# Kernel optimization log

Measured on AMD Instinct MI355X. Metric: run time of the kernel, lower is better.

The kernel has to match this reference:

```python
import jax, jax.numpy as jnp
import numpy as np

N, E, B = 100000, 400000, 4096      # nodes, directed edges, graphs
P, d = 4, 49                        # phm_dim, per-component dim; D = P*d = 196
L = 3                               # message-passing layers
D1, D2 = 64, 32                     # downstream per-component dims (256/4, 128/4)


def setup_inputs():
    key = jax.random.key(0)
    ks = jax.random.split(key, 20)
    def nrm(k, shape, s=0.1):
        return jax.random.normal(k, shape, dtype=jnp.float32) * s
    return {
        "x": jax.random.randint(ks[0], (N, 9), 0, 119),
        "edge_index": jax.random.randint(ks[1], (2, E), 0, N),
        "edge_attr": jax.random.randint(ks[2], (E, 3), 0, 8),
        "batch": jnp.sort(jax.random.randint(ks[3], (N,), 0, B)),
        # encoders: summed categorical embeddings in hypercomplex form [*, P, d]
        "atom_emb": nrm(ks[4], (9, 119, P, d)),
        "bond_emb": nrm(ks[5], (L, 3, 8, P, d)),
        # per-layer PHM conv: contribution matrices A (phm rule) + component weights W
        "conv_A": nrm(ks[6], (L, P, P, P), 0.5),
        "conv_W": nrm(ks[7], (L, P, d, d)),
        "conv_b": jnp.zeros((L, P, d), jnp.float32),
        "mp_gamma": jnp.ones((L, P * d), jnp.float32),
        "mp_beta": jnp.zeros((L, P * d), jnp.float32),
        # soft-attention pooling: PHM linear + real transformer gate
        "pool_A": nrm(ks[8], (P, P, P), 0.5),
        "pool_W": nrm(ks[9], (P, d, d)),
        "pool_b": jnp.zeros((P, d), jnp.float32),
        "pool_rt_w": nrm(ks[10], (P,), 0.5),
        "pool_rt_b": jnp.zeros((d,), jnp.float32),
        # downstream PHM MLP 196 -> 256 -> 128 -> 4*1, then real trafo -> 1
        "dn_A": nrm(ks[11], (3, P, P, P), 0.5),
        "dn1_W": nrm(ks[12], (P, d, D1)),
        "dn1_b": jnp.zeros((P, D1), jnp.float32),
        "dn1_gamma": jnp.ones((P * D1,), jnp.float32),
        "dn1_beta": jnp.zeros((P * D1,), jnp.float32),
        "dn2_W": nrm(ks[13], (P, D1, D2)),
        "dn2_b": jnp.zeros((P, D2), jnp.float32),
        "dn2_gamma": jnp.ones((P * D2,), jnp.float32),
        "dn2_beta": jnp.zeros((P * D2,), jnp.float32),
        "dn3_W": nrm(ks[14], (P, D2, 1)),
        "dn3_b": jnp.zeros((P, 1), jnp.float32),
        "rt_w": nrm(ks[15], (P,), 0.5),
        "rt_b": jnp.zeros((1,), jnp.float32),
    }


def phm_linear(x, A, W, b):
    # PHM linear: y = x @ (sum_i kron(A_i, W_i)) + b, on [n, P, din] -> [n, P, dout]
    return jnp.einsum('nkp,ikj,ipq->njq', x, A, W) + b


def naive_bn(x, gamma, beta, eps=1e-5):
    # naive batch norm over the batch axis, per flattened hypercomplex feature
    n, p, dd = x.shape
    x2 = x.reshape(n, p * dd)
    mu = x2.mean(axis=0)
    var = x2.var(axis=0)
    x2 = (x2 - mu) * jax.lax.rsqrt(var + eps) * gamma + beta
    return x2.reshape(n, p, dd)


def reference(x, edge_index, edge_attr, batch, atom_emb, bond_emb,
              conv_A, conv_W, conv_b, mp_gamma, mp_beta,
              pool_A, pool_W, pool_b, pool_rt_w, pool_rt_b,
              dn_A, dn1_W, dn1_b, dn1_gamma, dn1_beta,
              dn2_W, dn2_b, dn2_gamma, dn2_beta, dn3_W, dn3_b, rt_w, rt_b):
    src, dst = edge_index[0], edge_index[1]
    # atom encoder: sum embeddings of 9 categorical features -> [N, P, d]
    h0 = atom_emb[jnp.arange(9), x].sum(axis=1)
    h = h0
    for l in range(L):  # small fixed layer count
        # bond encoder for this layer -> [E, P, d]
        e = bond_emb[l][jnp.arange(3), edge_attr].sum(axis=1)
        # message = x_j + e_ij (identity msg encoder); self-loop (zero edge feat) adds h
        m = h[src] + e
        agg = jax.ops.segment_sum(m, dst, num_segments=N) + h
        z = phm_linear(agg, conv_A[l], conv_W[l], conv_b[l])
        z = jax.nn.relu(naive_bn(z, mp_gamma[l], mp_beta[l]))
        h = z + h0  # skip-connect to first embedding (sc_type='first')
    # soft-attention pooling: real-valued sigmoid gate per node feature
    g = jax.nn.sigmoid(
        jnp.einsum('npk,p->nk', phm_linear(h, pool_A, pool_W, pool_b), pool_rt_w)
        + pool_rt_b)
    pooled = jax.ops.segment_sum(h * g[:, None, :], batch, num_segments=B)  # [B, P, d]
    # downstream PHM MLP with naive batch norm + relu
    z = jax.nn.relu(naive_bn(phm_linear(pooled, dn_A[0], dn1_W, dn1_b), dn1_gamma, dn1_beta))
    z = jax.nn.relu(naive_bn(phm_linear(z, dn_A[1], dn2_W, dn2_b), dn2_gamma, dn2_beta))
    o = phm_linear(z, dn_A[2], dn3_W, dn3_b)          # [B, P, 1]
    return jnp.einsum('npk,p->nk', o, rt_w) + rt_b    # [B, 1]
```

## Files before the change

### kernel.cpp

```cpp
#include <hip/hip_runtime.h>
#include <cstdint>
#include <cstddef>

#define N_NODES 100000
#define N_EDGES 400000
#define N_GRAPHS 4096
#define DF 196
#define DD 49
#define NPB 5
#define TST 200
#define WSLOT 14336
#define EST 232

#define AS1 __attribute__((address_space(1)))
#define AS3 __attribute__((address_space(3)))

typedef __bf16 bf16x8 __attribute__((ext_vector_type(8)));
typedef float f32x4 __attribute__((ext_vector_type(4)));

__device__ __forceinline__ unsigned short f2bf(float f) {
  unsigned int u = __float_as_uint(f);
  u = u + 0x7FFFu + ((u >> 16) & 1u);
  return (unsigned short)(u >> 16);
}
__device__ __forceinline__ float bf2f(unsigned short h) {
  return __uint_as_float(((unsigned int)h) << 16);
}

__global__ void convert_wfrag_kernel(const float* __restrict__ cA,
                                     const float* __restrict__ cW,
                                     unsigned short* __restrict__ wfrag) {
  int idx = blockIdx.x * blockDim.x + threadIdx.x;
  if (idx >= 3 * 100352) return;
  int l = idx / 100352;
  int r = idx - l * 100352;
  int ct = r / 7168; int r1 = r - ct * 7168;
  int ks = r1 / 1024; int r2 = r1 - ks * 1024;
  int h = r2 / 512;  int r3 = r2 - h * 512;
  int ln = r3 / 8;   int j = r3 - ln * 8;
  int col = ct * 16 + (ln & 15);
  int k = ks * 32 + (ln >> 4) * 8 + j;
  float v = 0.f;
  if (col < DF && k < DF) {
    int k4 = k / DD, p = k - (k / DD) * DD;
    int j4 = col / DD, q = col - (col / DD) * DD;
#pragma unroll
    for (int i = 0; i < 4; i++)
      v += cA[((l * 4 + i) * 4 + k4) * 4 + j4] * cW[((l * 4 + i) * DD + p) * DD + q];
  }
  unsigned short hi = f2bf(v);
  wfrag[idx] = (h == 0) ? hi : f2bf(v - bf2f(hi));
}

__global__ void setup_small_kernel(const float* __restrict__ bond, float* __restrict__ lut,
                                   const float* __restrict__ pA, const float* __restrict__ pW,
                                   const float* __restrict__ pb, const float* __restrict__ rtw,
                                   const float* __restrict__ rtb,
                                   float* __restrict__ gateW, float* __restrict__ gbias,
                                   const float* __restrict__ dnA,
                                   const float* __restrict__ W1, const float* __restrict__ W2,
                                   const float* __restrict__ W3,
                                   float* __restrict__ M1, float* __restrict__ M2,
                                   float* __restrict__ M3) {
  int idx0 = blockIdx.x * blockDim.x + threadIdx.x;
  const int NL = 3 * 512 * DF;
  const int NG = DF * DD + DD;
  const int n1 = DF * 256, n2 = 256 * 128, n3 = 128 * 4;
  if (idx0 < NL) {
    int idx = idx0;
    int l = idx / (512 * DF);
    int r = idx - l * (512 * DF);
    int code = r / DF, c = r - (r / DF) * DF;
    int a0 = code & 7, a1 = (code >> 3) & 7, a2 = (code >> 6) & 7;
    lut[idx] = bond[((l * 3 + 0) * 8 + a0) * DF + c]
             + bond[((l * 3 + 1) * 8 + a1) * DF + c]
             + bond[((l * 3 + 2) * 8 + a2) * DF + c];
  } else if (idx0 < NL + NG) {
    int idx = idx0 - NL;
    if (idx < DF * DD) {
      int r = idx / DD, q = idx - (idx / DD) * DD;
      int k = r / DD, p = r - (r / DD) * DD;
      float s = 0.f;
#pragma unroll
      for (int i = 0; i < 4; i++) {
        float aw = 0.f;
#pragma unroll
        for (int j = 0; j < 4; j++) aw += pA[(i * 4 + k) * 4 + j] * rtw[j];
        s += aw * pW[(i * DD + p) * DD + q];
      }
      gateW[idx] = s;
    } else {
      int q = idx - DF * DD;
      float s = rtb[q];
#pragma unroll
      for (int j = 0; j < 4; j++) s += rtw[j] * pb[j * DD + q];
      gbias[q] = s;
    }
  } else if (idx0 < NL + NG + n1 + n2 + n3) {
    int idx = idx0 - NL - NG;
    if (idx < n1) {
      int r = idx >> 8, c = idx & 255;
      int k = r / DD, p = r - (r / DD) * DD;
      int j = c >> 6, Q = c & 63;
      float s = 0.f;
#pragma unroll
      for (int i = 0; i < 4; i++) s += dnA[i * 16 + k * 4 + j] * W1[(i * DD + p) * 64 + Q];
      M1[idx] = s;
    } else if (idx < n1 + n2) {
      int m = idx - n1;
      int r = m >> 7, c = m & 127;
      int k = r >> 6, p = r & 63, j = c >> 5, q = c & 31;
      float s = 0.f;
#pragma unroll
      for (int i = 0; i < 4; i++) s += dnA[64 + i * 16 + k * 4 + j] * W2[(i * 64 + p) * 32 + q];
      M2[m] = s;
    } else {
      int m = idx - n1 - n2;
      int r = m >> 2, j = m & 3;
      int k = r >> 5, p = r & 31;
      float s = 0.f;
#pragma unroll
      for (int i = 0; i < 4; i++) s += dnA[128 + i * 16 + k * 4 + j] * W3[i * 32 + p];
      M3[m] = s;
    }
  }
}

__global__ void hist_kernel(const int* __restrict__ dst, int* __restrict__ counts) {
  int e = blockIdx.x * blockDim.x + threadIdx.x;
  if (e < N_EDGES) atomicAdd(&counts[dst[e]], 1);
}

__global__ void scan_local_kernel(const int* __restrict__ counts, int* __restrict__ offs,
                                  int* __restrict__ bsum) {
  __shared__ int sm[256];
  int tid = threadIdx.x;
  int gid = blockIdx.x * 256 + tid;
  int v = (gid < N_NODES) ? counts[gid] : 0;
  sm[tid] = v;
  __syncthreads();
  for (int d = 1; d < 256; d <<= 1) {
    int add = (tid >= d) ? sm[tid - d] : 0;
    __syncthreads();
    sm[tid] += add;
    __syncthreads();
  }
  if (gid < N_NODES) offs[gid] = sm[tid] - v;
  if (tid == 255) bsum[blockIdx.x] = sm[255];
}

__global__ void scan_bsum_kernel(int* __restrict__ bsum, int* __restrict__ bpre, int nb) {
  __shared__ int sm[512];
  int tid = threadIdx.x;
  int v = (tid < nb) ? bsum[tid] : 0;
  sm[tid] = v;
  __syncthreads();
  for (int d = 1; d < 512; d <<= 1) {
    int add = (tid >= d) ? sm[tid - d] : 0;
    __syncthreads();
    sm[tid] += add;
    __syncthreads();
  }
  if (tid < nb) bpre[tid] = sm[tid] - v;
}

__global__ void add_off_kernel(int* __restrict__ offs, const int* __restrict__ bpre) {
  int gid = blockIdx.x * blockDim.x + threadIdx.x;
  if (gid < N_NODES) offs[gid] += bpre[gid >> 8];
  if (gid == 0) offs[N_NODES] = N_EDGES;
}

__global__ void scatter_kernel(const int* __restrict__ src, const int* __restrict__ dst,
                               const int* __restrict__ ea, int* __restrict__ counts,
                               const int* __restrict__ offs,
                               unsigned int* __restrict__ sorted) {
  int e = blockIdx.x * blockDim.x + threadIdx.x;
  if (e >= N_EDGES) return;
  int d = dst[e];
  int code = ea[e * 3 + 0] | (ea[e * 3 + 1] << 3) | (ea[e * 3 + 2] << 6);
  int pos = offs[d] + atomicSub(&counts[d], 1) - 1;
  sorted[pos] = (unsigned int)src[e] | ((unsigned int)code << 17);
}

__global__ void sortseg_kernel(const int* __restrict__ offs,
                               unsigned int* __restrict__ sorted) {
  int n = blockIdx.x * blockDim.x + threadIdx.x;
  if (n >= N_NODES) return;
  int s = offs[n], e = offs[n + 1];
  for (int i = s + 1; i < e; i++) {
    unsigned int v = sorted[i];
    int j = i - 1;
    while (j >= s && sorted[j] > v) { sorted[j + 1] = sorted[j]; j--; }
    sorted[j + 1] = v;
  }
}

__global__ void atom_enc_kernel(const int* __restrict__ x, const float* __restrict__ emb,
                                float* __restrict__ h0) {
  int idx = blockIdx.x * blockDim.x + threadIdx.x;
  if (idx >= N_NODES * DF) return;
  int n = idx / DF;
  int c = idx - n * DF;
  float s = 0.f;
#pragma unroll
  for (int f = 0; f < 9; f++) {
    int xi = x[n * 9 + f];
    s += emb[(f * 119 + xi) * DF + c];
  }
  h0[idx] = s;
}

__global__ __launch_bounds__(256)
void agg_kernel(const float* __restrict__ h, const int* __restrict__ offs,
                const unsigned int* __restrict__ sorted, const float* __restrict__ lut,
                unsigned short* __restrict__ tH, unsigned short* __restrict__ tL) {
  int t = threadIdx.x;
  int i = t / 49, q = t - i * 49;
  if (i >= NPB) return;
  int node = blockIdx.x * NPB + i;
  if (node >= N_NODES) return;
  const float4* h4 = (const float4*)h;
  const float4* l4 = (const float4*)lut;
  float4 acc = h4[(size_t)node * 49 + q];
  int s = offs[node], e = offs[node + 1];
  for (int k = s; k < e; k++) {
    unsigned int se = sorted[k];
    int srcn = se & 0x1FFFF;
    int code = se >> 17;
    float4 hv = h4[(size_t)srcn * 49 + q];
    float4 lv = l4[(size_t)code * 49 + q];
    acc.x += hv.x + lv.x;
    acc.y += hv.y + lv.y;
    acc.z += hv.z + lv.z;
    acc.w += hv.w + lv.w;
  }
  ushort4 hh, ll;
  hh.x = f2bf(acc.x); ll.x = f2bf(acc.x - bf2f(hh.x));
  hh.y = f2bf(acc.y); ll.y = f2bf(acc.y - bf2f(hh.y));
  hh.z = f2bf(acc.z); ll.z = f2bf(acc.z - bf2f(hh.z));
  hh.w = f2bf(acc.w); ll.w = f2bf(acc.w - bf2f(hh.w));
  size_t ob = (size_t)node * TST + q * 4;
  *(ushort4*)(tH + ob) = hh;
  *(ushort4*)(tL + ob) = ll;
  if (q == 48) {
    ushort4 z = make_ushort4(0, 0, 0, 0);
    *(ushort4*)(tH + (size_t)node * TST + 196) = z;
    *(ushort4*)(tL + (size_t)node * TST + 196) = z;
  }
}

__global__ __launch_bounds__(256, 2)
void conv_mfma_kernel(unsigned short* __restrict__ tH,
                      unsigned short* __restrict__ tL,
                      const unsigned short* __restrict__ wfrag,
                      const float* __restrict__ bias,
                      float* __restrict__ stats) {
  __shared__ __align__(16) unsigned short smW[2 * 64 * EST];
  const int t = threadIdx.x;
  const int lane = t & 63;
  const int w = t >> 6;
  const int li = lane & 15;
  const int rg = lane >> 4;
  const int rowbase = blockIdx.x * 128 + w * 32;

  f32x4 acc[2][14];
#pragma unroll
  for (int rt = 0; rt < 2; rt++)
#pragma unroll
    for (int ct = 0; ct < 14; ct++) acc[rt][ct] = (f32x4){0.f, 0.f, 0.f, 0.f};

  uint4 b0h[2], b0l[2], b1h[2], b1l[2], b2h[2], b2l[2], b3h[2], b3l[2];

#define LOADA(ks, aH, aL)                                                      \
  {                                                                            \
    _Pragma("unroll") for (int rt = 0; rt < 2; rt++) {                         \
      size_t o = (size_t)(rowbase + rt * 16 + li) * TST + (ks) * 32 + rg * 8;  \
      aH[rt] = *(const uint4*)(tH + o);                                        \
      aL[rt] = *(const uint4*)(tL + o);                                        \
    }                                                                          \
  }

#define WLOAD(ks, sbase)                                                       \
  {                                                                            \
    _Pragma("unroll") for (int f0 = 0; f0 < 7; f0++) {                         \
      int g = f0 * 4 + w;                                                      \
      int hh = g & 1, ct = g >> 1;                                             \
      __builtin_amdgcn_global_load_lds(                                        \
          (AS1 const void*)(wfrag + ((size_t)(ct * 7 + (ks)) * 2 + hh) * 512 + lane * 8), \
          (AS3 void*)(smW + (sbase) + (ct * 2 + hh) * 512), 16, 0, 0);         \
    }                                                                          \
  }

#define COMPUTE(sbase, aH, aL)                                                 \
  {                                                                            \
    _Pragma("unroll") for (int ct = 0; ct < 14; ct++) {                        \
      bf16x8 bh = *(const bf16x8*)(smW + (sbase) + ((ct * 2 + 0) * 512 + lane * 8)); \
      bf16x8 bl = *(const bf16x8*)(smW + (sbase) + ((ct * 2 + 1) * 512 + lane * 8)); \
      _Pragma("unroll") for (int rt = 0; rt < 2; rt++) {                       \
        bf16x8 ah = *(const bf16x8*)&aH[rt];                                   \
        bf16x8 al = *(const bf16x8*)&aL[rt];                                   \
        acc[rt][ct] = __builtin_amdgcn_mfma_f32_16x16x32_bf16(ah, bh, acc[rt][ct], 0, 0, 0); \
        acc[rt][ct] = __builtin_amdgcn_mfma_f32_16x16x32_bf16(al, bh, acc[rt][ct], 0, 0, 0); \
        acc[rt][ct] = __builtin_amdgcn_mfma_f32_16x16x32_bf16(ah, bl, acc[rt][ct], 0, 0, 0); \
      }                                                                        \
    }                                                                          \
  }

#define BARC(N)                                                                \
  {                                                                            \
    asm volatile("s_waitcnt vmcnt(" #N ")" ::: "memory");                      \
    __builtin_amdgcn_s_barrier();                                              \
  }
#define PINW() __builtin_amdgcn_sched_barrier(0)

  WLOAD(0, 0);
  PINW();
  LOADA(0, b0h, b0l);
  LOADA(1, b1h, b1l);
  LOADA(2, b2h, b2l);
  BARC(12);
  WLOAD(1, WSLOT); PINW(); LOADA(3, b3h, b3l); COMPUTE(0, b0h, b0l);     BARC(4);
  WLOAD(2, 0);     PINW(); LOADA(4, b0h, b0l); COMPUTE(WSLOT, b1h, b1l); BARC(4);
  WLOAD(3, WSLOT); PINW(); LOADA(5, b1h, b1l); COMPUTE(0, b2h, b2l);     BARC(4);
  WLOAD(4, 0);     PINW(); LOADA(6, b2h, b2l); COMPUTE(WSLOT, b3h, b3l); BARC(4);
  WLOAD(5, WSLOT); PINW();                     COMPUTE(0, b0h, b0l);     BARC(0);
  WLOAD(6, 0);     PINW();                     COMPUTE(WSLOT, b1h, b1l); BARC(0);
  COMPUTE(0, b2h, b2l);

  float part[14], psq[14];
#pragma unroll
  for (int ct = 0; ct < 14; ct++) { part[ct] = 0.f; psq[ct] = 0.f; }

  unsigned short* lhi = smW;
  unsigned short* llo = smW + 64 * EST;

#pragma unroll
  for (int half = 0; half < 2; half++) {
    __syncthreads();
    if ((w >> 1) == half) {
      int rl0 = (w & 1) * 32;
#pragma unroll
      for (int ct = 0; ct < 14; ct++) {
        int c = ct * 16 + li;
        float bv = (c < DF) ? bias[c] : 0.f;
#pragma unroll
        for (int rt = 0; rt < 2; rt++) {
#pragma unroll
          for (int r = 0; r < 4; r++) {
            int row = rl0 + rt * 16 + rg * 4 + r;
            int gr = rowbase + rt * 16 + rg * 4 + r;
            float y = acc[rt][ct][r] + bv;
            if (gr < N_NODES && c < DF) { part[ct] += y; psq[ct] += y * y; }
            unsigned short hi = f2bf(y);
            lhi[row * EST + c] = hi;
            llo[row * EST + c] = f2bf(y - bf2f(hi));
          }
        }
      }
    }
    __syncthreads();
    for (int idx = t; idx < 1600; idx += 256) {
      int row = idx / 25, u = idx - (idx / 25) * 25;
      int gr = blockIdx.x * 128 + half * 64 + row;
      if (gr < N_NODES) {
        uint4 vh = *(const uint4*)(lhi + row * EST + u * 8);
        uint4 vl = *(const uint4*)(llo + row * EST + u * 8);
        if (u == 24) { vh.z = 0u; vh.w = 0u; vl.z = 0u; vl.w = 0u; }
        *(uint4*)(tH + (size_t)gr * TST + u * 8) = vh;
        *(uint4*)(tL + (size_t)gr * TST + u * 8) = vl;
      }
    }
  }

  __syncthreads();
  float* redS = (float*)smW;
  float* redQ = redS + 4 * 224;
#pragma unroll
  for (int ct = 0; ct < 14; ct++) {
    float p = part[ct], q = psq[ct];
    p += __shfl_xor(p, 16, 64); p += __shfl_xor(p, 32, 64);
    q += __shfl_xor(q, 16, 64); q += __shfl_xor(q, 32, 64);
    if (rg == 0) { redS[w * 224 + ct * 16 + li] = p; redQ[w * 224 + ct * 16 + li] = q; }
  }
  __syncthreads();
  if (t < DF) {
    float s1 = redS[t] + redS[224 + t] + redS[448 + t] + redS[672 + t];
    float s2 = redQ[t] + redQ[224 + t] + redQ[448 + t] + redQ[672 + t];
    atomicAdd(&stats[t], s1);
    atomicAdd(&stats[DF + t], s2);
  }
#undef LOADA
#undef WLOAD
#undef COMPUTE
#undef BARC
#undef PINW
}

__global__ void bn_relu_split_kernel(const unsigned short* __restrict__ tH,
                                     const unsigned short* __restrict__ tL,
                                     const float* __restrict__ stats,
                                     const float* __restrict__ gamma,
                                     const float* __restrict__ beta,
                                     const float* __restrict__ h0,
                                     float* __restrict__ h) {
  int idx = blockIdx.x * blockDim.x + threadIdx.x;
  if (idx >= N_NODES * DD) return;
  int n = idx / DD, q = idx - (idx / DD) * DD;
  size_t ib = (size_t)n * TST + q * 4;
  ushort4 hv = *(const ushort4*)(tH + ib);
  ushort4 lv = *(const ushort4*)(tL + ib);
  size_t fb = (size_t)n * DF + q * 4;
  float4 sk = *(const float4*)(h0 + fb);
  int c = q * 4;
  const float invN = 1.f / N_NODES;
  float4 o;
  {
    float z = bf2f(hv.x) + bf2f(lv.x);
    float mu = stats[c + 0] * invN;
    float var = stats[DF + c + 0] * invN - mu * mu;
    o.x = fmaxf((z - mu) * rsqrtf(var + 1e-5f) * gamma[c + 0] + beta[c + 0], 0.f) + sk.x;
  }
  {
    float z = bf2f(hv.y) + bf2f(lv.y);
    float mu = stats[c + 1] * invN;
    float var = stats[DF + c + 1] * invN - mu * mu;
    o.y = fmaxf((z - mu) * rsqrtf(var + 1e-5f) * gamma[c + 1] + beta[c + 1], 0.f) + sk.y;
  }
  {
    float z = bf2f(hv.z) + bf2f(lv.z);
    float mu = stats[c + 2] * invN;
    float var = stats[DF + c + 2] * invN - mu * mu;
    o.z = fmaxf((z - mu) * rsqrtf(var + 1e-5f) * gamma[c + 2] + beta[c + 2], 0.f) + sk.z;
  }
  {
    float z = bf2f(hv.w) + bf2f(lv.w);
    float mu = stats[c + 3] * invN;
    float var = stats[DF + c + 3] * invN - mu * mu;
    o.w = fmaxf((z - mu) * rsqrtf(var + 1e-5f) * gamma[c + 3] + beta[c + 3], 0.f) + sk.w;
  }
  *(float4*)(h + fb) = o;
}

template<int S, int MODE>
__launch_bounds__(256)
__global__ void gemm_kernel(const float* X, const float* __restrict__ W,
                            const float* __restrict__ bias, float* Y,
                            float* __restrict__ stats, int Nrows, int K, int NC) {
  constexpr int WN = S * 64;
  __shared__ __align__(16) float At[32][64];
  __shared__ __align__(16) float Wl[32][WN];
  const int t = threadIdx.x;
  const int tx = t & 15;
  const int ty = t >> 4;
  const int r0 = blockIdx.x * 64;

  float acc[S][4][4];
#pragma unroll
  for (int s = 0; s < S; s++)
#pragma unroll
    for (int i = 0; i < 4; i++)
#pragma unroll
      for (int j = 0; j < 4; j++) acc[s][i][j] = 0.f;

  const int lr = t >> 2;
  const int kb = (t & 3) * 8;
  constexpr int TPR = S * 16;
  const int cw = (t % TPR) * 4;
  const int kr = t / TPR;
  constexpr int RPP = 256 / TPR;
  constexpr int PASSES = 32 / RPP;

  for (int k0 = 0; k0 < K; k0 += 32) {
    {
      const int gr = r0 + lr;
      const float* xp = X + (size_t)gr * K + k0 + kb;
      if (gr < Nrows && (k0 + kb + 7) < K) {
        float4 v0 = *(const float4*)(xp);
        float4 v1 = *(const float4*)(xp + 4);
        At[kb + 0][lr] = v0.x; At[kb + 1][lr] = v0.y;
        At[kb + 2][lr] = v0.z; At[kb + 3][lr] = v0.w;
        At[kb + 4][lr] = v1.x; At[kb + 5][lr] = v1.y;
        At[kb + 6][lr] = v1.z; At[kb + 7][lr] = v1.w;
      } else {
#pragma unroll
        for (int i = 0; i < 8; i++) {
          int kk = kb + i;
          float v = 0.f;
          if (gr < Nrows && (k0 + kk) < K) v = xp[i];
          At[kk][lr] = v;
        }
      }
    }
#pragma unroll
    for (int ps = 0; ps < PASSES; ps++) {
      int kk = kr + ps * RPP;
      int gk = k0 + kk;
      if (gk < K && (cw + 3) < NC && ((NC & 3) == 0)) {
        float4 v = *(const float4*)(W + (size_t)gk * NC + cw);
        Wl[kk][cw + 0] = v.x; Wl[kk][cw + 1] = v.y;
        Wl[kk][cw + 2] = v.z; Wl[kk][cw + 3] = v.w;
      } else {
#pragma unroll
        for (int j = 0; j < 4; j++) {
          int c = cw + j;
          float v = 0.f;
          if (gk < K && c < NC) v = W[(size_t)gk * NC + c];
          Wl[kk][c] = v;
        }
      }
    }
    __syncthreads();
#pragma unroll 4
    for (int kk = 0; kk < 32; kk++) {
      float4 a = *(const float4*)&At[kk][ty * 4];
      float av[4] = {a.x, a.y, a.z, a.w};
#pragma unroll
      for (int s = 0; s < S; s++) {
        float4 w = *(const float4*)&Wl[kk][s * 64 + tx * 4];
        float wv[4] = {w.x, w.y, w.z, w.w};
#pragma unroll
        for (int i = 0; i < 4; i++)
#pragma unroll
          for (int j = 0; j < 4; j++)
            acc[s][i][j] = fmaf(av[i], wv[j], acc[s][i][j]);
      }
    }
    __syncthreads();
  }

#pragma unroll
  for (int s = 0; s < S; s++)
#pragma unroll
    for (int j = 0; j < 4; j++) {
      int c = s * 64 + tx * 4 + j;
      float bv = (c < NC) ? bias[c] : 0.f;
#pragma unroll
      for (int i = 0; i < 4; i++) {
        float y = acc[s][i][j] + bv;
        if (MODE == 1) y = 1.f / (1.f + __expf(-y));
        acc[s][i][j] = y;
      }
    }
#pragma unroll
  for (int i = 0; i < 4; i++) {
    int gr = r0 + ty * 4 + i;
    if (gr < Nrows) {
#pragma unroll
      for (int s = 0; s < S; s++)
#pragma unroll
        for (int j = 0; j < 4; j++) {
          int c = s * 64 + tx * 4 + j;
          if (c < NC) Y[(size_t)gr * NC + c] = acc[s][i][j];
        }
    }
  }
  if (MODE == 0) {
    float* red = &Wl[0][0];
    __syncthreads();
#pragma unroll
    for (int s = 0; s < S; s++)
#pragma unroll
      for (int j = 0; j < 4; j++) {
        float p = 0.f;
#pragma unroll
        for (int i = 0; i < 4; i++)
          if ((r0 + ty * 4 + i) < Nrows) p += acc[s][i][j];
        red[ty * WN + s * 64 + tx * 4 + j] = p;
      }
    __syncthreads();
    if (t < WN) {
      float tot = 0.f;
#pragma unroll
      for (int yy = 0; yy < 16; yy++) tot += red[yy * WN + t];
      if (t < NC) atomicAdd(&stats[t], tot);
    }
    __syncthreads();
#pragma unroll
    for (int s = 0; s < S; s++)
#pragma unroll
      for (int j = 0; j < 4; j++) {
        float p = 0.f;
#pragma unroll
        for (int i = 0; i < 4; i++)
          if ((r0 + ty * 4 + i) < Nrows) p += acc[s][i][j] * acc[s][i][j];
        red[ty * WN + s * 64 + tx * 4 + j] = p;
      }
    __syncthreads();
    if (t < WN) {
      float tot = 0.f;
#pragma unroll
      for (int yy = 0; yy < 16; yy++) tot += red[yy * WN + t];
      if (t < NC) atomicAdd(&stats[NC + t], tot);
    }
  }
}

__global__ void bn_relu_kernel(const float* __restrict__ z, const float* __restrict__ stats,
                               const float* __restrict__ gamma, const float* __restrict__ beta,
                               float* __restrict__ out,
                               int total, int NC, float invN) {
  int idx = blockIdx.x * blockDim.x + threadIdx.x;
  if (idx >= total) return;
  int c = idx % NC;
  float mu = stats[c] * invN;
  float var = stats[NC + c] * invN - mu * mu;
  float v = (z[idx] - mu) * rsqrtf(var + 1e-5f) * gamma[c] + beta[c];
  out[idx] = fmaxf(v, 0.f);
}

__device__ __forceinline__ int lower_bound_dev(const int* a, int n, int v) {
  int lo = 0, hi = n;
  while (lo < hi) { int mid = (lo + hi) >> 1; if (a[mid] < v) lo = mid + 1; else hi = mid; }
  return lo;
}

__global__ void pool_kernel(const float* __restrict__ h, const float* __restrict__ g,
                            const int* __restrict__ batch, float* __restrict__ pooled) {
  int b = blockIdx.x;
  __shared__ int bounds[2];
  if (threadIdx.x == 0) {
    bounds[0] = lower_bound_dev(batch, N_NODES, b);
    bounds[1] = lower_bound_dev(batch, N_NODES, b + 1);
  }
  __syncthreads();
  int c = threadIdx.x;
  if (c >= DF) return;
  int s = bounds[0], e = bounds[1];
  int q = c % DD;
  float acc = 0.f;
  for (int n = s; n < e; n++)
    acc = fmaf(h[(size_t)n * DF + c], g[(size_t)n * DD + q], acc);
  pooled[(size_t)b * DF + c] = acc;
}

__global__ void final_kernel(const float* __restrict__ z2, const float* __restrict__ M3,
                             const float* __restrict__ b3, const float* __restrict__ rtw,
                             const float* __restrict__ rtb, float* __restrict__ out) {
  __shared__ float sM[128 * 4];
  __shared__ float srw[4];
  __shared__ float srb;
  int t = threadIdx.x;
  for (int i = t; i < 512; i += 256) sM[i] = M3[i];
  if (t < 4) srw[t] = rtw[t];
  if (t == 4) srb = rtb[0];
  __syncthreads();
  int b = blockIdx.x * blockDim.x + t;
  if (b >= N_GRAPHS) return;
  float o0 = b3[0], o1 = b3[1], o2 = b3[2], o3 = b3[3];
  const float* zp = z2 + (size_t)b * 128;
  for (int p = 0; p < 128; p++) {
    float v = zp[p];
    o0 = fmaf(v, sM[p * 4 + 0], o0);
    o1 = fmaf(v, sM[p * 4 + 1], o1);
    o2 = fmaf(v, sM[p * 4 + 2], o2);
    o3 = fmaf(v, sM[p * 4 + 3], o3);
  }
  out[b] = srb + o0 * srw[0] + o1 * srw[1] + o2 * srw[2] + o3 * srw[3];
}

extern "C" void kernel_launch(void* const* d_in, const int* in_sizes, int n_in,
                              void* d_out, int out_size, void* d_ws, size_t ws_size,
                              hipStream_t stream) {
  (void)in_sizes; (void)n_in; (void)out_size; (void)ws_size;
  const int* x          = (const int*)d_in[0];
  const int* edge_index = (const int*)d_in[1];
  const int* edge_attr  = (const int*)d_in[2];
  const int* batch      = (const int*)d_in[3];
  const float* atom_emb = (const float*)d_in[4];
  const float* bond_emb = (const float*)d_in[5];
  const float* conv_A   = (const float*)d_in[6];
  const float* conv_W   = (const float*)d_in[7];
  const float* conv_b   = (const float*)d_in[8];
  const float* mp_gamma = (const float*)d_in[9];
  const float* mp_beta  = (const float*)d_in[10];
  const float* pool_A   = (const float*)d_in[11];
  const float* pool_W   = (const float*)d_in[12];
  const float* pool_b   = (const float*)d_in[13];
  const float* pool_rt_w = (const float*)d_in[14];
  const float* pool_rt_b = (const float*)d_in[15];
  const float* dn_A     = (const float*)d_in[16];
  const float* dn1_W    = (const float*)d_in[17];
  const float* dn1_b    = (const float*)d_in[18];
  const float* dn1_gamma = (const float*)d_in[19];
  const float* dn1_beta = (const float*)d_in[20];
  const float* dn2_W    = (const float*)d_in[21];
  const float* dn2_b    = (const float*)d_in[22];
  const float* dn2_gamma = (const float*)d_in[23];
  const float* dn2_beta = (const float*)d_in[24];
  const float* dn3_W    = (const float*)d_in[25];
  const float* dn3_b    = (const float*)d_in[26];
  const float* rt_w     = (const float*)d_in[27];
  const float* rt_b     = (const float*)d_in[28];
  float* out = (float*)d_out;

  char* ws = (char*)d_ws;
  size_t off = 0;
  auto alloc = [&](size_t bytes) -> char* {
    char* p = ws + off;
    off = (off + bytes + 255) & ~(size_t)255;
    return p;
  };
  const size_t HBYTES = (size_t)N_NODES * DF * sizeof(float);
  float* h0 = (float*)alloc(HBYTES);
  float* h  = (float*)alloc(HBYTES);
  unsigned short* tH = (unsigned short*)alloc((size_t)N_NODES * TST * 2 + 4096);
  unsigned short* tL = (unsigned short*)alloc((size_t)N_NODES * TST * 2 + 4096);
  float* g      = (float*)tH;
  float* pooled = (float*)((char*)tH + (((size_t)N_NODES * DD * 4 + 255) & ~(size_t)255));
  float* z1     = (float*)((char*)pooled + (((size_t)N_GRAPHS * DF * 4 + 255) & ~(size_t)255));
  float* z2     = (float*)((char*)z1 + (((size_t)N_GRAPHS * 256 * 4 + 255) & ~(size_t)255));
  unsigned short* wfrag = (unsigned short*)alloc((size_t)3 * 100352 * 2);
  float* gateW  = (float*)alloc(DF * DD * 4);
  float* gbias  = (float*)alloc(64 * 4);
  float* M1     = (float*)alloc(DF * 256 * 4);
  float* M2     = (float*)alloc(256 * 128 * 4);
  float* M3     = (float*)alloc(128 * 4 * 4);
  float* stats  = (float*)alloc(2048 * 4);
  int*  counts  = (int*)alloc(N_NODES * 4);
  int*  offs    = (int*)alloc((N_NODES + 1) * 4);
  unsigned int* sorted = (unsigned int*)alloc((size_t)N_EDGES * 4);
  float* lut    = (float*)alloc((size_t)3 * 512 * DF * 4);
  int*  bsum    = (int*)alloc(512 * 4);
  int*  bpre    = (int*)alloc(512 * 4);

  const int* src = edge_index;
  const int* dst = edge_index + N_EDGES;
  const int NB = (N_NODES + 255) / 256;

  hipMemsetAsync(stats, 0, 2048 * 4, stream);
  hipMemsetAsync(counts, 0, N_NODES * 4, stream);

  convert_wfrag_kernel<<<(3 * 100352 + 255) / 256, 256, 0, stream>>>(conv_A, conv_W, wfrag);
  {
    const int total = 3 * 512 * DF + (DF * DD + DD) + (DF * 256 + 256 * 128 + 128 * 4);
    setup_small_kernel<<<(total + 255) / 256, 256, 0, stream>>>(
        bond_emb, lut, pool_A, pool_W, pool_b, pool_rt_w, pool_rt_b, gateW, gbias,
        dn_A, dn1_W, dn2_W, dn3_W, M1, M2, M3);
  }

  hist_kernel<<<(N_EDGES + 255) / 256, 256, 0, stream>>>(dst, counts);
  scan_local_kernel<<<NB, 256, 0, stream>>>(counts, offs, bsum);
  scan_bsum_kernel<<<1, 512, 0, stream>>>(bsum, bpre, NB);
  add_off_kernel<<<NB, 256, 0, stream>>>(offs, bpre);
  scatter_kernel<<<(N_EDGES + 255) / 256, 256, 0, stream>>>(
      src, dst, edge_attr, counts, offs, sorted);
  sortseg_kernel<<<NB, 256, 0, stream>>>(offs, sorted);

  atom_enc_kernel<<<(N_NODES * DF + 255) / 256, 256, 0, stream>>>(x, atom_emb, h0);

  const int NCONV = (N_NODES + 127) / 128;
  for (int l = 0; l < 3; l++) {
    const float* hl = (l == 0) ? h0 : h;
    agg_kernel<<<(N_NODES + NPB - 1) / NPB, 256, 0, stream>>>(
        hl, offs, sorted, lut + (size_t)l * 512 * DF, tH, tL);
    float* st = stats + l * 392;
    conv_mfma_kernel<<<NCONV, 256, 0, stream>>>(
        tH, tL, wfrag + (size_t)l * 100352, conv_b + (size_t)l * DF, st);
    bn_relu_split_kernel<<<(N_NODES * DD + 255) / 256, 256, 0, stream>>>(
        tH, tL, st, mp_gamma + l * DF, mp_beta + l * DF, h0, h);
  }

  gemm_kernel<1, 1><<<(N_NODES + 63) / 64, 256, 0, stream>>>(
      h, gateW, gbias, g, nullptr, N_NODES, DF, DD);
  pool_kernel<<<N_GRAPHS, 256, 0, stream>>>(h, g, batch, pooled);

  gemm_kernel<4, 0><<<(N_GRAPHS + 63) / 64, 256, 0, stream>>>(
      pooled, M1, dn1_b, z1, stats + 1176, N_GRAPHS, DF, 256);
  bn_relu_kernel<<<(N_GRAPHS * 256 + 255) / 256, 256, 0, stream>>>(
      z1, stats + 1176, dn1_gamma, dn1_beta, z1, N_GRAPHS * 256, 256, 1.f / N_GRAPHS);
  gemm_kernel<2, 0><<<(N_GRAPHS + 63) / 64, 256, 0, stream>>>(
      z1, M2, dn2_b, z2, stats + 1688, N_GRAPHS, 256, 128);
  bn_relu_kernel<<<(N_GRAPHS * 128 + 255) / 256, 256, 0, stream>>>(
      z2, stats + 1688, dn2_gamma, dn2_beta, z2, N_GRAPHS * 128, 128, 1.f / N_GRAPHS);
  final_kernel<<<(N_GRAPHS + 255) / 256, 256, 0, stream>>>(z2, M3, dn3_b, rt_w, rt_b, out);
}
```

Measured before the change: 885.1 us.

## Compute attention gate with split-bf16 MFMA kernel fed by fused BN output

```diff
diff --git a/kernel.cpp b/kernel.cpp
--- a/kernel.cpp
+++ b/kernel.cpp
@@ -56,7 +56,8 @@
                                    const float* __restrict__ pA, const float* __restrict__ pW,
                                    const float* __restrict__ pb, const float* __restrict__ rtw,
                                    const float* __restrict__ rtb,
-                                   float* __restrict__ gateW, float* __restrict__ gbias,
+                                   unsigned short* __restrict__ wfragG,
+                                   float* __restrict__ gbias,
                                    const float* __restrict__ dnA,
                                    const float* __restrict__ W1, const float* __restrict__ W2,
                                    const float* __restrict__ W3,
@@ -64,7 +65,8 @@
                                    float* __restrict__ M3) {
   int idx0 = blockIdx.x * blockDim.x + threadIdx.x;
   const int NL = 3 * 512 * DF;
-  const int NG = DF * DD + DD;
+  const int NGF = 28672;
+  const int NB2 = 64;
   const int n1 = DF * 256, n2 = 256 * 128, n3 = 128 * 4;
   if (idx0 < NL) {
     int idx = idx0;
@@ -75,29 +77,37 @@
     lut[idx] = bond[((l * 3 + 0) * 8 + a0) * DF + c]
              + bond[((l * 3 + 1) * 8 + a1) * DF + c]
              + bond[((l * 3 + 2) * 8 + a2) * DF + c];
-  } else if (idx0 < NL + NG) {
+  } else if (idx0 < NL + NGF) {
     int idx = idx0 - NL;
-    if (idx < DF * DD) {
-      int r = idx / DD, q = idx - (idx / DD) * DD;
-      int k = r / DD, p = r - (r / DD) * DD;
-      float s = 0.f;
+    int ct = idx / 7168; int r1 = idx - ct * 7168;
+    int ks = r1 / 1024; int r2 = r1 - ks * 1024;
+    int h = r2 / 512;  int r3 = r2 - h * 512;
+    int ln = r3 / 8;   int j = r3 - ln * 8;
+    int col = ct * 16 + (ln & 15);
+    int k = ks * 32 + (ln >> 4) * 8 + j;
+    float v = 0.f;
+    if (col < DD && k < DF) {
+      int kp = k / DD, p = k - (k / DD) * DD;
 #pragma unroll
       for (int i = 0; i < 4; i++) {
         float aw = 0.f;
 #pragma unroll
-        for (int j = 0; j < 4; j++) aw += pA[(i * 4 + k) * 4 + j] * rtw[j];
-        s += aw * pW[(i * DD + p) * DD + q];
-      }
-      gateW[idx] = s;
-    } else {
-      int q = idx - DF * DD;
+        for (int j4 = 0; j4 < 4; j4++) aw += pA[(i * 4 + kp) * 4 + j4] * rtw[j4];
+        v += aw * pW[(i * DD + p) * DD + col];
+      }
+    }
+    unsigned short hi = f2bf(v);
+    wfragG[idx] = (h == 0) ? hi : f2bf(v - bf2f(hi));
+  } else if (idx0 < NL + NGF + NB2) {
+    int q = idx0 - NL - NGF;
+    if (q < DD) {
       float s = rtb[q];
 #pragma unroll
       for (int j = 0; j < 4; j++) s += rtw[j] * pb[j * DD + q];
       gbias[q] = s;
     }
-  } else if (idx0 < NL + NG + n1 + n2 + n3) {
-    int idx = idx0 - NL - NG;
+  } else if (idx0 < NL + NGF + NB2 + n1 + n2 + n3) {
+    int idx = idx0 - NL - NGF - NB2;
     if (idx < n1) {
       int r = idx >> 8, c = idx & 255;
       int k = r / DD, p = r - (r / DD) * DD;
@@ -396,13 +406,13 @@
 #undef PINW
 }
 
-__global__ void bn_relu_split_kernel(const unsigned short* __restrict__ tH,
-                                     const unsigned short* __restrict__ tL,
+__global__ void bn_relu_split_kernel(unsigned short* __restrict__ tH,
+                                     unsigned short* __restrict__ tL,
                                      const float* __restrict__ stats,
                                      const float* __restrict__ gamma,
                                      const float* __restrict__ beta,
                                      const float* __restrict__ h0,
-                                     float* __restrict__ h) {
+                                     float* __restrict__ h, int write_split) {
   int idx = blockIdx.x * blockDim.x + threadIdx.x;
   if (idx >= N_NODES * DD) return;
   int n = idx / DD, q = idx - (idx / DD) * DD;
@@ -439,6 +449,97 @@
     o.w = fmaxf((z - mu) * rsqrtf(var + 1e-5f) * gamma[c + 3] + beta[c + 3], 0.f) + sk.w;
   }
   *(float4*)(h + fb) = o;
+  if (write_split) {
+    ushort4 sh, sl;
+    sh.x = f2bf(o.x); sl.x = f2bf(o.x - bf2f(sh.x));
+    sh.y = f2bf(o.y); sl.y = f2bf(o.y - bf2f(sh.y));
+    sh.z = f2bf(o.z); sl.z = f2bf(o.z - bf2f(sh.z));
+    sh.w = f2bf(o.w); sl.w = f2bf(o.w - bf2f(sh.w));
+    *(ushort4*)(tH + ib) = sh;
+    *(ushort4*)(tL + ib) = sl;
+  }
+}
+
+__global__ __launch_bounds__(256, 2)
+void gate_mfma_kernel(const unsigned short* __restrict__ tH,
+                      const unsigned short* __restrict__ tL,
+                      const unsigned short* __restrict__ wfragG,
+                      const float* __restrict__ gbias,
+                      float* __restrict__ g) {
+  __shared__ __align__(16) unsigned short smW[28672];
+  const int t = threadIdx.x;
+  const int lane = t & 63;
+  const int w = t >> 6;
+  const int li = lane & 15;
+  const int rg = lane >> 4;
+  const int rowbase = blockIdx.x * 128 + w * 32;
+
+  f32x4 acc[2][4];
+#pragma unroll
+  for (int rt = 0; rt < 2; rt++)
+#pragma unroll
+    for (int ct = 0; ct < 4; ct++) acc[rt][ct] = (f32x4){0.f, 0.f, 0.f, 0.f};
+
+  uint4 b0h[2], b0l[2], b1h[2], b1l[2], b2h[2], b2l[2], b3h[2], b3l[2];
+
+#define LOADA(ks, aH, aL)                                                      \
+  {                                                                            \
+    _Pragma("unroll") for (int rt = 0; rt < 2; rt++) {                         \
+      size_t o = (size_t)(rowbase + rt * 16 + li) * TST + (ks) * 32 + rg * 8;  \
+      aH[rt] = *(const uint4*)(tH + o);                                        \
+      aL[rt] = *(const uint4*)(tL + o);                                        \
+    }                                                                          \
+  }
+
+#define COMPUTE(ks, aH, aL)                                                    \
+  {                                                                            \
+    _Pragma("unroll") for (int ct = 0; ct < 4; ct++) {                         \
+      bf16x8 bh = *(const bf16x8*)(smW + ((ct * 7 + (ks)) * 2 + 0) * 512 + lane * 8); \
+      bf16x8 bl = *(const bf16x8*)(smW + ((ct * 7 + (ks)) * 2 + 1) * 512 + lane * 8); \
+      _Pragma("unroll") for (int rt = 0; rt < 2; rt++) {                       \
+        bf16x8 ah = *(const bf16x8*)&aH[rt];                                   \
+        bf16x8 al = *(const bf16x8*)&aL[rt];                                   \
+        acc[rt][ct] = __builtin_amdgcn_mfma_f32_16x16x32_bf16(ah, bh, acc[rt][ct], 0, 0, 0); \
+        acc[rt][ct] = __builtin_amdgcn_mfma_f32_16x16x32_bf16(al, bh, acc[rt][ct], 0, 0, 0); \
+        acc[rt][ct] = __builtin_amdgcn_mfma_f32_16x16x32_bf16(ah, bl, acc[rt][ct], 0, 0, 0); \
+      }                                                                        \
+    }                                                                          \
+  }
+
+  LOADA(0, b0h, b0l);
+  LOADA(1, b1h, b1l);
+  LOADA(2, b2h, b2l);
+  for (int i = t; i < 3584; i += 256)
+    *(uint4*)(smW + (size_t)i * 8) = *(const uint4*)(wfragG + (size_t)i * 8);
+  __syncthreads();
+  LOADA(3, b3h, b3l); COMPUTE(0, b0h, b0l);
+  LOADA(4, b0h, b0l); COMPUTE(1, b1h, b1l);
+  LOADA(5, b1h, b1l); COMPUTE(2, b2h, b2l);
+  LOADA(6, b2h, b2l); COMPUTE(3, b3h, b3l);
+  COMPUTE(4, b0h, b0l);
+  COMPUTE(5, b1h, b1l);
+  COMPUTE(6, b2h, b2l);
+
+#pragma unroll
+  for (int ct = 0; ct < 4; ct++) {
+    int c = ct * 16 + li;
+    if (c < DD) {
+      float bv = gbias[c];
+#pragma unroll
+      for (int rt = 0; rt < 2; rt++) {
+#pragma unroll
+        for (int r = 0; r < 4; r++) {
+          int gr = rowbase + rt * 16 + rg * 4 + r;
+          if (gr < N_NODES) {
+            float v = acc[rt][ct][r] + bv;
+            g[(size_t)gr * DD + c] = 1.f / (1.f + __expf(-v));
+          }
+        }
+      }
+    }
+  }
+#undef LOADA
+#undef COMPUTE
 }
 
 template<int S, int MODE>
@@ -705,12 +806,12 @@
   float* h  = (float*)alloc(HBYTES);
   unsigned short* tH = (unsigned short*)alloc((size_t)N_NODES * TST * 2 + 4096);
   unsigned short* tL = (unsigned short*)alloc((size_t)N_NODES * TST * 2 + 4096);
-  float* g      = (float*)tH;
-  float* pooled = (float*)((char*)tH + (((size_t)N_NODES * DD * 4 + 255) & ~(size_t)255));
+  float* g      = (float*)h0;
+  float* pooled = (float*)((char*)h0 + (((size_t)N_NODES * DD * 4 + 255) & ~(size_t)255));
   float* z1     = (float*)((char*)pooled + (((size_t)N_GRAPHS * DF * 4 + 255) & ~(size_t)255));
   float* z2     = (float*)((char*)z1 + (((size_t)N_GRAPHS * 256 * 4 + 255) & ~(size_t)255));
   unsigned short* wfrag = (unsigned short*)alloc((size_t)3 * 100352 * 2);
-  float* gateW  = (float*)alloc(DF * DD * 4);
+  unsigned short* wfragG = (unsigned short*)alloc((size_t)28672 * 2);
   float* gbias  = (float*)alloc(64 * 4);
   float* M1     = (float*)alloc(DF * 256 * 4);
   float* M2     = (float*)alloc(256 * 128 * 4);
@@ -732,9 +833,9 @@
 
   convert_wfrag_kernel<<<(3 * 100352 + 255) / 256, 256, 0, stream>>>(conv_A, conv_W, wfrag);
   {
-    const int total = 3 * 512 * DF + (DF * DD + DD) + (DF * 256 + 256 * 128 + 128 * 4);
+    const int total = 3 * 512 * DF + 28672 + 64 + (DF * 256 + 256 * 128 + 128 * 4);
     setup_small_kernel<<<(total + 255) / 256, 256, 0, stream>>>(
-        bond_emb, lut, pool_A, pool_W, pool_b, pool_rt_w, pool_rt_b, gateW, gbias,
+        bond_emb, lut, pool_A, pool_W, pool_b, pool_rt_w, pool_rt_b, wfragG, gbias,
         dn_A, dn1_W, dn2_W, dn3_W, M1, M2, M3);
   }
 
@@ -757,11 +858,10 @@
     conv_mfma_kernel<<<NCONV, 256, 0, stream>>>(
         tH, tL, wfrag + (size_t)l * 100352, conv_b + (size_t)l * DF, st);
     bn_relu_split_kernel<<<(N_NODES * DD + 255) / 256, 256, 0, stream>>>(
-        tH, tL, st, mp_gamma + l * DF, mp_beta + l * DF, h0, h);
-  }
-
-  gemm_kernel<1, 1><<<(N_NODES + 63) / 64, 256, 0, stream>>>(
-      h, gateW, gbias, g, nullptr, N_NODES, DF, DD);
+        tH, tL, st, mp_gamma + l * DF, mp_beta + l * DF, h0, h, (l == 2) ? 1 : 0);
+  }
+
+  gate_mfma_kernel<<<NCONV, 256, 0, stream>>>(tH, tL, wfragG, gbias, g);
   pool_kernel<<<N_GRAPHS, 256, 0, stream>>>(h, g, batch, pooled);
 
   gemm_kernel<4, 0><<<(N_GRAPHS + 63) / 64, 256, 0, stream>>>(
```

Result: no change. 875.8 us (-1.1%).
